# Kernel optimization log

Measured on AMD Instinct MI355X. Metric: run time of the kernel, lower is better.

Reference implementation:

```python
import jax, jax.numpy as jnp
import numpy as np

B, N, IN_DIM, OUT_DIM, C = 8, 8192, 1024, 512, 64
TEMPERATURE = 1.0
LN_EPS = 1e-5


def setup_inputs() -> dict:
    key = jax.random.key(0)
    ks = jax.random.split(key, 6)
    node_embeddings = jax.random.normal(ks[0], (B, N, IN_DIM), dtype=jnp.float32)
    node_mask = jnp.zeros((B, N), dtype=bool)  # True => node is masked out
    # xavier_uniform for cluster_centers [C, OUT_DIM]
    lim_c = float(np.sqrt(6.0 / (C + OUT_DIM)))
    cluster_centers = jax.random.uniform(ks[1], (C, OUT_DIM), jnp.float32, -lim_c, lim_c)
    # nn.Linear default init (kaiming-uniform-ish bounds)
    lim_n = float(1.0 / np.sqrt(IN_DIM))
    W_node = jax.random.uniform(ks[2], (IN_DIM, OUT_DIM), jnp.float32, -lim_n, lim_n)
    b_node = jax.random.uniform(ks[3], (OUT_DIM,), jnp.float32, -lim_n, lim_n)
    lim_k = float(1.0 / np.sqrt(OUT_DIM))
    W_cluster = jax.random.uniform(ks[4], (OUT_DIM, OUT_DIM), jnp.float32, -lim_k, lim_k)
    b_cluster = jax.random.uniform(ks[5], (OUT_DIM,), jnp.float32, -lim_k, lim_k)
    ln_gamma = jnp.ones((OUT_DIM,), jnp.float32)
    ln_beta = jnp.zeros((OUT_DIM,), jnp.float32)
    return {
        "node_embeddings": node_embeddings,
        "node_mask": node_mask,
        "cluster_centers": cluster_centers,
        "W_node": W_node,
        "b_node": b_node,
        "W_cluster": W_cluster,
        "b_cluster": b_cluster,
        "ln_gamma": ln_gamma,
        "ln_beta": ln_beta,
    }


def reference(node_embeddings, node_mask, cluster_centers, W_node, b_node,
              W_cluster, b_cluster, ln_gamma, ln_beta):
    # node projection: [B, N, D]
    node_proj = jnp.einsum('bni,io->bno', node_embeddings, W_node) + b_node
    # projected cluster centers (batch-independent): [C, D]
    ccp = cluster_centers @ W_cluster + b_cluster
    # similarities: [B, C, N]
    sims = jnp.einsum('cd,bnd->bcn', ccp, node_proj) / TEMPERATURE
    sims = jnp.where(node_mask[:, None, :], -jnp.inf, sims)
    assignment_weights = jax.nn.softmax(sims, axis=-1)  # dropout is identity in eval
    # aggregate: [B, C, D], residual add of projected centers
    compressed = jnp.einsum('bcn,bnd->bcd', assignment_weights, node_proj) + ccp
    # LayerNorm over last dim
    mu = jnp.mean(compressed, axis=-1, keepdims=True)
    var = jnp.var(compressed, axis=-1, keepdims=True)
    compressed = (compressed - mu) * jax.lax.rsqrt(var + LN_EPS) * ln_gamma + ln_beta
    return compressed, assignment_weights
```

## Files before the change

### kernel.cpp

```cpp
#include <hip/hip_runtime.h>
#include <hip/hip_bf16.h>
#include <math.h>

#define Bn 8
#define Nn 8192
#define KIN 1024
#define DOUT 512
#define NC 64
#define LN_EPS 1e-5f

typedef short bf16x8 __attribute__((ext_vector_type(8)));
typedef short s4v __attribute__((ext_vector_type(4)));
typedef short s8v __attribute__((ext_vector_type(8)));
typedef float f32x4 __attribute__((ext_vector_type(4)));

__device__ __forceinline__ short f2bf(float f) {
    __hip_bfloat16 h = __float2bfloat16(f);
    return __builtin_bit_cast(short, h);
}

__device__ __forceinline__ void load_lds16(const void* g, void* l) {
    __builtin_amdgcn_global_load_lds(
        (const __attribute__((address_space(1))) unsigned int*)g,
        (__attribute__((address_space(3))) unsigned int*)l, 16, 0, 0);
}

__global__ void k_prep_w(const float* __restrict__ W, short* __restrict__ Wt) {
    int o = blockIdx.x * 256 + threadIdx.x;
    int n = o >> 10, k = o & 1023;
    Wt[o] = f2bf(W[k * DOUT + n]);
}

__global__ void k_prep_c(const float* __restrict__ cc, const float* __restrict__ Wc,
                         const float* __restrict__ bc, float* __restrict__ ccp_f,
                         short* __restrict__ ccp_bf) {
    int o = blockIdx.x * 256 + threadIdx.x;
    int c = o >> 9, n = o & 511;
    float a = bc[n];
    for (int k = 0; k < DOUT; ++k) a += cc[c * DOUT + k] * Wc[k * DOUT + n];
    ccp_f[o] = a;
    ccp_bf[o] = f2bf(a);
}

__global__ __launch_bounds__(512) void k_gemm1(
    const float* __restrict__ A, const short* __restrict__ Wt,
    const float* __restrict__ bias, short* __restrict__ proj) {
    __shared__ short As[64 * 32];
    __shared__ short Bs[512 * 32];
    const int tid = threadIdx.x;
    const int lane = tid & 63, wv = tid >> 6;
    const int quad = lane >> 4, l15 = lane & 15;
    const int m0 = blockIdx.x * 64;

    f32x4 acc[4][4];
#pragma unroll
    for (int i = 0; i < 4; ++i)
#pragma unroll
        for (int j = 0; j < 4; ++j) acc[i][j] = (f32x4){0.f, 0.f, 0.f, 0.f};

    const int ar = tid >> 3;
    const int akq = (tid & 7) * 4;
    const float* Ag = A + (size_t)(m0 + ar) * KIN + akq;

    for (int it = 0; it < KIN / 32; ++it) {
        __syncthreads();
        const int k0 = it * 32;
        {
            float4 av = *reinterpret_cast<const float4*>(Ag + k0);
            s4v pv;
            pv.x = f2bf(av.x); pv.y = f2bf(av.y); pv.z = f2bf(av.z); pv.w = f2bf(av.w);
            *reinterpret_cast<s4v*>(&As[ar * 32 + akq]) = pv;
        }
#pragma unroll
        for (int iss = 0; iss < 4; ++iss) {
            int c = iss * 512 + tid;
            int n = c >> 2, kc = c & 3;
            load_lds16(Wt + n * KIN + k0 + kc * 8, Bs + (iss * 512 + wv * 64) * 8);
        }
        __syncthreads();
        bf16x8 af[4], bfr[4];
#pragma unroll
        for (int mi = 0; mi < 4; ++mi)
            af[mi] = *reinterpret_cast<const bf16x8*>(&As[(mi * 16 + l15) * 32 + quad * 8]);
#pragma unroll
        for (int ni = 0; ni < 4; ++ni)
            bfr[ni] = *reinterpret_cast<const bf16x8*>(&Bs[(wv * 64 + ni * 16 + l15) * 32 + quad * 8]);
#pragma unroll
        for (int mi = 0; mi < 4; ++mi)
#pragma unroll
            for (int ni = 0; ni < 4; ++ni)
                acc[mi][ni] = __builtin_amdgcn_mfma_f32_16x16x32_bf16(af[mi], bfr[ni], acc[mi][ni], 0, 0, 0);
    }
#pragma unroll
    for (int ni = 0; ni < 4; ++ni) {
        int col = wv * 64 + ni * 16 + l15;
        float bv = bias[col];
#pragma unroll
        for (int mi = 0; mi < 4; ++mi)
#pragma unroll
            for (int r = 0; r < 4; ++r) {
                int row = m0 + mi * 16 + quad * 4 + r;
                proj[(size_t)row * DOUT + col] = f2bf(acc[mi][ni][r] + bv);
            }
    }
}

__global__ __launch_bounds__(256) void k_sims(
    const short* __restrict__ ccp_bf, const short* __restrict__ proj,
    float* __restrict__ sims) {
    __shared__ short As[64 * 32];
    __shared__ short Bs[128 * 32];
    const int tid = threadIdx.x, lane = tid & 63, wv = tid >> 6;
    const int quad = lane >> 4, l15 = lane & 15;
    const int b = blockIdx.x >> 6, nt = blockIdx.x & 63;
    const int n0 = nt * 128;
    const int wm = wv >> 1, wn = wv & 1;

    f32x4 acc[2][4];
#pragma unroll
    for (int i = 0; i < 2; ++i)
#pragma unroll
        for (int j = 0; j < 4; ++j) acc[i][j] = (f32x4){0.f, 0.f, 0.f, 0.f};

    for (int it = 0; it < DOUT / 32; ++it) {
        __syncthreads();
        const int k0 = it * 32;
        {
            int r = tid >> 2, kc = tid & 3;
            load_lds16(ccp_bf + r * DOUT + k0 + kc * 8, As + wv * 64 * 8);
        }
#pragma unroll
        for (int iss = 0; iss < 2; ++iss) {
            int c = iss * 256 + tid;
            int r = c >> 2, kc = c & 3;
            load_lds16(proj + (size_t)(b * Nn + n0 + r) * DOUT + k0 + kc * 8,
                       Bs + (iss * 256 + wv * 64) * 8);
        }
        __syncthreads();
        bf16x8 af[2], bfr[4];
#pragma unroll
        for (int mi = 0; mi < 2; ++mi)
            af[mi] = *reinterpret_cast<const bf16x8*>(&As[(wm * 32 + mi * 16 + l15) * 32 + quad * 8]);
#pragma unroll
        for (int ni = 0; ni < 4; ++ni)
            bfr[ni] = *reinterpret_cast<const bf16x8*>(&Bs[(wn * 64 + ni * 16 + l15) * 32 + quad * 8]);
#pragma unroll
        for (int mi = 0; mi < 2; ++mi)
#pragma unroll
            for (int ni = 0; ni < 4; ++ni)
                acc[mi][ni] = __builtin_amdgcn_mfma_f32_16x16x32_bf16(af[mi], bfr[ni], acc[mi][ni], 0, 0, 0);
    }
#pragma unroll
    for (int mi = 0; mi < 2; ++mi)
#pragma unroll
        for (int ni = 0; ni < 4; ++ni)
#pragma unroll
            for (int r = 0; r < 4; ++r) {
                int c = wm * 32 + mi * 16 + quad * 4 + r;
                int n = n0 + wn * 64 + ni * 16 + l15;
                sims[((size_t)b * NC + c) * Nn + n] = acc[mi][ni][r];
            }
}

__global__ __launch_bounds__(256) void k_softmax(
    float* __restrict__ aw, const unsigned char* __restrict__ mask,
    short* __restrict__ aw_bf) {
    __shared__ float red[8];
    const int tid = threadIdx.x, lane = tid & 63, wv = tid >> 6;
    const int b = blockIdx.x >> 6, c = blockIdx.x & 63;
    float* p = aw + ((size_t)b * NC + c) * Nn;
    short* q = aw_bf + ((size_t)b * NC + c) * Nn;
    const unsigned char* mp = mask + b * Nn;

    float v[32];
    float mx = -INFINITY;
#pragma unroll
    for (int i = 0; i < 32; ++i) {
        int idx = tid + i * 256;
        float x = p[idx];
        if (mp[idx]) x = -INFINITY;
        v[i] = x;
        mx = fmaxf(mx, x);
    }
    for (int off = 32; off; off >>= 1) mx = fmaxf(mx, __shfl_xor(mx, off));
    if (lane == 0) red[wv] = mx;
    __syncthreads();
    mx = fmaxf(fmaxf(red[0], red[1]), fmaxf(red[2], red[3]));
    __syncthreads();

    float s = 0.f;
#pragma unroll
    for (int i = 0; i < 32; ++i) {
        v[i] = expf(v[i] - mx);
        s += v[i];
    }
    for (int off = 32; off; off >>= 1) s += __shfl_xor(s, off);
    if (lane == 0) red[wv] = s;
    __syncthreads();
    s = red[0] + red[1] + red[2] + red[3];
    float inv = 1.f / s;
#pragma unroll
    for (int i = 0; i < 32; ++i) {
        int idx = tid + i * 256;
        float w = v[i] * inv;
        p[idx] = w;
        q[idx] = f2bf(w);
    }
}

__global__ __launch_bounds__(256) void k_agg(
    const short* __restrict__ aw_bf, const short* __restrict__ proj,
    float* __restrict__ partial) {
    __shared__ short As[64 * 32];
    __shared__ short Bs[64 * 40];
    const int tid = threadIdx.x, lane = tid & 63, wv = tid >> 6;
    const int quad = lane >> 4, l15 = lane & 15;
    const int b = blockIdx.x >> 6, dt = (blockIdx.x >> 3) & 7, ks = blockIdx.x & 7;
    const int d0 = dt * 64;
    const int wc = wv >> 1, wd = wv & 1;

    f32x4 acc[2][2];
#pragma unroll
    for (int i = 0; i < 2; ++i)
#pragma unroll
        for (int j = 0; j < 2; ++j) acc[i][j] = (f32x4){0.f, 0.f, 0.f, 0.f};

    const int bk = tid >> 3;
    const int bj0 = (tid & 7) * 8;

    for (int it = 0; it < 32; ++it) {
        const int nb = ks * 1024 + it * 32;
        __syncthreads();
        {
            int r = tid >> 2, kc = tid & 3;
            load_lds16(aw_bf + ((size_t)b * NC + r) * Nn + nb + kc * 8, As + wv * 64 * 8);
        }
        {
            const short* g = proj + (size_t)(b * Nn + nb + bk) * DOUT + d0 + bj0;
            s8v x = *reinterpret_cast<const s8v*>(g);
#pragma unroll
            for (int j = 0; j < 8; ++j) Bs[(bj0 + j) * 40 + bk] = x[j];
        }
        __syncthreads();
        bf16x8 af[2], bfr[2];
#pragma unroll
        for (int ci = 0; ci < 2; ++ci)
            af[ci] = *reinterpret_cast<const bf16x8*>(&As[(wc * 32 + ci * 16 + l15) * 32 + quad * 8]);
#pragma unroll
        for (int di = 0; di < 2; ++di)
            bfr[di] = *reinterpret_cast<const bf16x8*>(&Bs[(wd * 32 + di * 16 + l15) * 40 + quad * 8]);
#pragma unroll
        for (int ci = 0; ci < 2; ++ci)
#pragma unroll
            for (int di = 0; di < 2; ++di)
                acc[ci][di] = __builtin_amdgcn_mfma_f32_16x16x32_bf16(af[ci], bfr[di], acc[ci][di], 0, 0, 0);
    }
#pragma unroll
    for (int ci = 0; ci < 2; ++ci)
#pragma unroll
        for (int di = 0; di < 2; ++di)
#pragma unroll
            for (int r = 0; r < 4; ++r) {
                int c = wc * 32 + ci * 16 + quad * 4 + r;
                int d = d0 + wd * 32 + di * 16 + l15;
                partial[(((size_t)b * 8 + ks) * NC + c) * DOUT + d] = acc[ci][di][r];
            }
}

__global__ __launch_bounds__(256) void k_ln(
    const float* __restrict__ partial, const float* __restrict__ ccp,
    const float* __restrict__ gamma, const float* __restrict__ beta,
    float* __restrict__ out) {
    __shared__ float red[16];
    const int tid = threadIdx.x, lane = tid & 63, wv = tid >> 6;
    const int b = blockIdx.x >> 6, c = blockIdx.x & 63;
    float v0 = ccp[c * DOUT + tid], v1 = ccp[c * DOUT + tid + 256];
#pragma unroll
    for (int ks = 0; ks < 8; ++ks) {
        const float* pp = partial + (((size_t)b * 8 + ks) * NC + c) * DOUT;
        v0 += pp[tid];
        v1 += pp[tid + 256];
    }
    float s = v0 + v1, sq = v0 * v0 + v1 * v1;
    for (int off = 32; off; off >>= 1) {
        s += __shfl_xor(s, off);
        sq += __shfl_xor(sq, off);
    }
    if (lane == 0) { red[wv] = s; red[8 + wv] = sq; }
    __syncthreads();
    s = red[0] + red[1] + red[2] + red[3];
    sq = red[8] + red[9] + red[10] + red[11];
    float mu = s * (1.f / 512.f);
    float var = sq * (1.f / 512.f) - mu * mu;
    float rs = rsqrtf(var + LN_EPS);
    size_t base = ((size_t)b * NC + c) * DOUT;
    out[base + tid] = (v0 - mu) * rs * gamma[tid] + beta[tid];
    out[base + tid + 256] = (v1 - mu) * rs * gamma[tid + 256] + beta[tid + 256];
}

extern "C" void kernel_launch(void* const* d_in, const int* in_sizes, int n_in,
                              void* d_out, int out_size, void* d_ws, size_t ws_size,
                              hipStream_t stream) {
    const float* node_emb = (const float*)d_in[0];
    const unsigned char* mask = (const unsigned char*)d_in[1];
    const float* cc = (const float*)d_in[2];
    const float* Wn = (const float*)d_in[3];
    const float* bn = (const float*)d_in[4];
    const float* Wc = (const float*)d_in[5];
    const float* bc = (const float*)d_in[6];
    const float* gamma = (const float*)d_in[7];
    const float* beta = (const float*)d_in[8];
    float* out = (float*)d_out;

    char* ws = (char*)d_ws;
    short* proj   = (short*)(ws);
    short* Wt     = (short*)(ws + 67108864);
    float* ccp_f  = (float*)(ws + 68157440);
    short* ccp_bf = (short*)(ws + 68288512);
    short* aw_bf  = (short*)(ws + 68354048);
    float* partial= (float*)(ws + 76742656);

    float* sims = out + (size_t)Bn * NC * DOUT;

    k_prep_w<<<2048, 256, 0, stream>>>(Wn, Wt);
    k_prep_c<<<128, 256, 0, stream>>>(cc, Wc, bc, ccp_f, ccp_bf);
    k_gemm1<<<1024, 512, 0, stream>>>(node_emb, Wt, bn, proj);
    k_sims<<<512, 256, 0, stream>>>(ccp_bf, proj, sims);
    k_softmax<<<512, 256, 0, stream>>>(sims, mask, aw_bf);
    k_agg<<<512, 256, 0, stream>>>(aw_bf, proj, partial);
    k_ln<<<512, 256, 0, stream>>>(partial, ccp_f, gamma, beta, out);
}
```

Baseline: 579.9 us.

## Retile projection GEMM, widen sims tiles, pre-transpose proj for aggregation

The projection GEMM moves from 64-row blocks covering all 512 outputs to 128x128 tiles with padded A rows in LDS. The sims kernel doubles its node tile to 256 with 512 threads. A new transpose kernel writes proj in d-major order so the aggregation kernel can use direct global-to-LDS loads with a 64-wide k step and 16-way split-K instead of scalar transposed LDS stores. This costs an extra 64 MB round trip through memory for projT and more partial sums to reduce in the LayerNorm kernel.

```diff
diff --git a/kernel.cpp b/kernel.cpp
--- a/kernel.cpp
+++ b/kernel.cpp
@@ -10,7 +10,6 @@
 #define LN_EPS 1e-5f
 
 typedef short bf16x8 __attribute__((ext_vector_type(8)));
-typedef short s4v __attribute__((ext_vector_type(4)));
 typedef short s8v __attribute__((ext_vector_type(8)));
 typedef float f32x4 __attribute__((ext_vector_type(4)));
 
@@ -42,15 +41,16 @@
     ccp_bf[o] = f2bf(a);
 }
 
-__global__ __launch_bounds__(512) void k_gemm1(
+__global__ __launch_bounds__(256) void k_gemm1(
     const float* __restrict__ A, const short* __restrict__ Wt,
     const float* __restrict__ bias, short* __restrict__ proj) {
-    __shared__ short As[64 * 32];
-    __shared__ short Bs[512 * 32];
-    const int tid = threadIdx.x;
-    const int lane = tid & 63, wv = tid >> 6;
+    __shared__ short As[128 * 40];
+    __shared__ short Bs[128 * 32];
+    const int tid = threadIdx.x, lane = tid & 63, wv = tid >> 6;
     const int quad = lane >> 4, l15 = lane & 15;
-    const int m0 = blockIdx.x * 64;
+    const int mt = blockIdx.x >> 2, nt = blockIdx.x & 3;
+    const int m0 = mt * 128, n0 = nt * 128;
+    const int wm = wv >> 1, wn = wv & 1;
 
     f32x4 acc[4][4];
 #pragma unroll
@@ -58,33 +58,41 @@
 #pragma unroll
         for (int j = 0; j < 4; ++j) acc[i][j] = (f32x4){0.f, 0.f, 0.f, 0.f};
 
-    const int ar = tid >> 3;
-    const int akq = (tid & 7) * 4;
-    const float* Ag = A + (size_t)(m0 + ar) * KIN + akq;
+    const int ar = tid >> 1;
+    const int ac = (tid & 1) * 16;
+    const float* Ag = A + (size_t)(m0 + ar) * KIN + ac;
 
     for (int it = 0; it < KIN / 32; ++it) {
-        __syncthreads();
         const int k0 = it * 32;
+        __syncthreads();
         {
-            float4 av = *reinterpret_cast<const float4*>(Ag + k0);
-            s4v pv;
-            pv.x = f2bf(av.x); pv.y = f2bf(av.y); pv.z = f2bf(av.z); pv.w = f2bf(av.w);
-            *reinterpret_cast<s4v*>(&As[ar * 32 + akq]) = pv;
-        }
-#pragma unroll
-        for (int iss = 0; iss < 4; ++iss) {
-            int c = iss * 512 + tid;
+            float4 a0 = *reinterpret_cast<const float4*>(Ag + k0);
+            float4 a1 = *reinterpret_cast<const float4*>(Ag + k0 + 4);
+            float4 a2 = *reinterpret_cast<const float4*>(Ag + k0 + 8);
+            float4 a3 = *reinterpret_cast<const float4*>(Ag + k0 + 12);
+            s8v p0, p1;
+            p0[0]=f2bf(a0.x); p0[1]=f2bf(a0.y); p0[2]=f2bf(a0.z); p0[3]=f2bf(a0.w);
+            p0[4]=f2bf(a1.x); p0[5]=f2bf(a1.y); p0[6]=f2bf(a1.z); p0[7]=f2bf(a1.w);
+            p1[0]=f2bf(a2.x); p1[1]=f2bf(a2.y); p1[2]=f2bf(a2.z); p1[3]=f2bf(a2.w);
+            p1[4]=f2bf(a3.x); p1[5]=f2bf(a3.y); p1[6]=f2bf(a3.z); p1[7]=f2bf(a3.w);
+            *reinterpret_cast<s8v*>(&As[ar * 40 + ac]) = p0;
+            *reinterpret_cast<s8v*>(&As[ar * 40 + ac + 8]) = p1;
+        }
+#pragma unroll
+        for (int i = 0; i < 2; ++i) {
+            int c = i * 256 + tid;
             int n = c >> 2, kc = c & 3;
-            load_lds16(Wt + n * KIN + k0 + kc * 8, Bs + (iss * 512 + wv * 64) * 8);
+            load_lds16(Wt + (size_t)(n0 + n) * KIN + k0 + kc * 8,
+                       Bs + (i * 256 + wv * 64) * 8);
         }
         __syncthreads();
         bf16x8 af[4], bfr[4];
 #pragma unroll
         for (int mi = 0; mi < 4; ++mi)
-            af[mi] = *reinterpret_cast<const bf16x8*>(&As[(mi * 16 + l15) * 32 + quad * 8]);
+            af[mi] = *reinterpret_cast<const bf16x8*>(&As[(wm * 64 + mi * 16 + l15) * 40 + quad * 8]);
 #pragma unroll
         for (int ni = 0; ni < 4; ++ni)
-            bfr[ni] = *reinterpret_cast<const bf16x8*>(&Bs[(wv * 64 + ni * 16 + l15) * 32 + quad * 8]);
+            bfr[ni] = *reinterpret_cast<const bf16x8*>(&Bs[(wn * 64 + ni * 16 + l15) * 32 + quad * 8]);
 #pragma unroll
         for (int mi = 0; mi < 4; ++mi)
 #pragma unroll
@@ -93,28 +101,28 @@
     }
 #pragma unroll
     for (int ni = 0; ni < 4; ++ni) {
-        int col = wv * 64 + ni * 16 + l15;
+        int col = n0 + wn * 64 + ni * 16 + l15;
         float bv = bias[col];
 #pragma unroll
         for (int mi = 0; mi < 4; ++mi)
 #pragma unroll
             for (int r = 0; r < 4; ++r) {
-                int row = m0 + mi * 16 + quad * 4 + r;
+                int row = m0 + wm * 64 + mi * 16 + quad * 4 + r;
                 proj[(size_t)row * DOUT + col] = f2bf(acc[mi][ni][r] + bv);
             }
     }
 }
 
-__global__ __launch_bounds__(256) void k_sims(
+__global__ __launch_bounds__(512) void k_sims(
     const short* __restrict__ ccp_bf, const short* __restrict__ proj,
     float* __restrict__ sims) {
     __shared__ short As[64 * 32];
-    __shared__ short Bs[128 * 32];
+    __shared__ short Bs[256 * 32];
     const int tid = threadIdx.x, lane = tid & 63, wv = tid >> 6;
     const int quad = lane >> 4, l15 = lane & 15;
-    const int b = blockIdx.x >> 6, nt = blockIdx.x & 63;
-    const int n0 = nt * 128;
-    const int wm = wv >> 1, wn = wv & 1;
+    const int b = blockIdx.x >> 5, nt = blockIdx.x & 31;
+    const int n0 = nt * 256;
+    const int wm = wv & 1, wn = wv >> 1;
 
     f32x4 acc[2][4];
 #pragma unroll
@@ -123,18 +131,18 @@
         for (int j = 0; j < 4; ++j) acc[i][j] = (f32x4){0.f, 0.f, 0.f, 0.f};
 
     for (int it = 0; it < DOUT / 32; ++it) {
-        __syncthreads();
         const int k0 = it * 32;
-        {
-            int r = tid >> 2, kc = tid & 3;
-            load_lds16(ccp_bf + r * DOUT + k0 + kc * 8, As + wv * 64 * 8);
-        }
-#pragma unroll
-        for (int iss = 0; iss < 2; ++iss) {
-            int c = iss * 256 + tid;
+        __syncthreads();
+        if (tid < 256) {
+            load_lds16(ccp_bf + (size_t)(tid >> 2) * DOUT + k0 + (tid & 3) * 8,
+                       As + (wv * 64) * 8);
+        }
+#pragma unroll
+        for (int i = 0; i < 2; ++i) {
+            int c = i * 512 + tid;
             int r = c >> 2, kc = c & 3;
             load_lds16(proj + (size_t)(b * Nn + n0 + r) * DOUT + k0 + kc * 8,
-                       Bs + (iss * 256 + wv * 64) * 8);
+                       Bs + (i * 512 + wv * 64) * 8);
         }
         __syncthreads();
         bf16x8 af[2], bfr[4];
@@ -208,62 +216,93 @@
     }
 }
 
+__global__ __launch_bounds__(256) void k_transpose(
+    const short* __restrict__ proj, short* __restrict__ projT) {
+    __shared__ short L[64 * 80];
+    const int tid = threadIdx.x;
+    const int nt = blockIdx.x >> 3, dt = blockIdx.x & 7;
+    {
+        int n = tid >> 2, d0 = (tid & 3) * 16;
+        const short* g = proj + (size_t)(nt * 64 + n) * DOUT + dt * 64 + d0;
+        s8v x0 = *reinterpret_cast<const s8v*>(g);
+        s8v x1 = *reinterpret_cast<const s8v*>(g + 8);
+        *reinterpret_cast<s8v*>(&L[n * 80 + d0]) = x0;
+        *reinterpret_cast<s8v*>(&L[n * 80 + d0 + 8]) = x1;
+    }
+    __syncthreads();
+    {
+        int d = tid & 63, n0 = (tid >> 6) * 16;
+        s8v y0, y1;
+#pragma unroll
+        for (int j = 0; j < 8; ++j) y0[j] = L[(n0 + j) * 80 + d];
+#pragma unroll
+        for (int j = 0; j < 8; ++j) y1[j] = L[(n0 + 8 + j) * 80 + d];
+        short* o = projT + (size_t)(dt * 64 + d) * (Bn * Nn) + nt * 64 + n0;
+        *reinterpret_cast<s8v*>(o) = y0;
+        *reinterpret_cast<s8v*>(o + 8) = y1;
+    }
+}
+
 __global__ __launch_bounds__(256) void k_agg(
-    const short* __restrict__ aw_bf, const short* __restrict__ proj,
+    const short* __restrict__ aw_bf, const short* __restrict__ projT,
     float* __restrict__ partial) {
-    __shared__ short As[64 * 32];
-    __shared__ short Bs[64 * 40];
+    __shared__ short As[64 * 64];
+    __shared__ short Bs[128 * 64];
     const int tid = threadIdx.x, lane = tid & 63, wv = tid >> 6;
     const int quad = lane >> 4, l15 = lane & 15;
-    const int b = blockIdx.x >> 6, dt = (blockIdx.x >> 3) & 7, ks = blockIdx.x & 7;
-    const int d0 = dt * 64;
-    const int wc = wv >> 1, wd = wv & 1;
-
-    f32x4 acc[2][2];
+    const int b = blockIdx.x >> 6, dt = (blockIdx.x >> 4) & 3, ks = blockIdx.x & 15;
+    const int d0 = dt * 128;
+    const int wm = wv >> 1, wn = wv & 1;
+
+    f32x4 acc[2][4];
 #pragma unroll
     for (int i = 0; i < 2; ++i)
 #pragma unroll
-        for (int j = 0; j < 2; ++j) acc[i][j] = (f32x4){0.f, 0.f, 0.f, 0.f};
-
-    const int bk = tid >> 3;
-    const int bj0 = (tid & 7) * 8;
-
-    for (int it = 0; it < 32; ++it) {
-        const int nb = ks * 1024 + it * 32;
-        __syncthreads();
-        {
-            int r = tid >> 2, kc = tid & 3;
-            load_lds16(aw_bf + ((size_t)b * NC + r) * Nn + nb + kc * 8, As + wv * 64 * 8);
-        }
-        {
-            const short* g = proj + (size_t)(b * Nn + nb + bk) * DOUT + d0 + bj0;
-            s8v x = *reinterpret_cast<const s8v*>(g);
-#pragma unroll
-            for (int j = 0; j < 8; ++j) Bs[(bj0 + j) * 40 + bk] = x[j];
-        }
-        __syncthreads();
-        bf16x8 af[2], bfr[2];
-#pragma unroll
-        for (int ci = 0; ci < 2; ++ci)
-            af[ci] = *reinterpret_cast<const bf16x8*>(&As[(wc * 32 + ci * 16 + l15) * 32 + quad * 8]);
-#pragma unroll
-        for (int di = 0; di < 2; ++di)
-            bfr[di] = *reinterpret_cast<const bf16x8*>(&Bs[(wd * 32 + di * 16 + l15) * 40 + quad * 8]);
-#pragma unroll
-        for (int ci = 0; ci < 2; ++ci)
-#pragma unroll
-            for (int di = 0; di < 2; ++di)
-                acc[ci][di] = __builtin_amdgcn_mfma_f32_16x16x32_bf16(af[ci], bfr[di], acc[ci][di], 0, 0, 0);
-    }
-#pragma unroll
-    for (int ci = 0; ci < 2; ++ci)
-#pragma unroll
-        for (int di = 0; di < 2; ++di)
+        for (int j = 0; j < 4; ++j) acc[i][j] = (f32x4){0.f, 0.f, 0.f, 0.f};
+
+    for (int it = 0; it < 8; ++it) {
+        const int nb = ks * 512 + it * 64;
+        __syncthreads();
+#pragma unroll
+        for (int i = 0; i < 2; ++i) {
+            int c = i * 256 + tid;
+            int r = c >> 3, kc = c & 7;
+            load_lds16(aw_bf + ((size_t)b * NC + r) * Nn + nb + kc * 8,
+                       As + (i * 256 + wv * 64) * 8);
+        }
+#pragma unroll
+        for (int i = 0; i < 4; ++i) {
+            int c = i * 256 + tid;
+            int r = c >> 3, kc = c & 7;
+            load_lds16(projT + (size_t)(d0 + r) * (Bn * Nn) + b * Nn + nb + kc * 8,
+                       Bs + (i * 256 + wv * 64) * 8);
+        }
+        __syncthreads();
+#pragma unroll
+        for (int k2 = 0; k2 < 2; ++k2) {
+            bf16x8 af[2], bfr[4];
+#pragma unroll
+            for (int mi = 0; mi < 2; ++mi)
+                af[mi] = *reinterpret_cast<const bf16x8*>(&As[(wm * 32 + mi * 16 + l15) * 64 + k2 * 32 + quad * 8]);
+#pragma unroll
+            for (int ni = 0; ni < 4; ++ni)
+                bfr[ni] = *reinterpret_cast<const bf16x8*>(&Bs[(wn * 64 + ni * 16 + l15) * 64 + k2 * 32 + quad * 8]);
+#pragma unroll
+            for (int mi = 0; mi < 2; ++mi)
+#pragma unroll
+                for (int ni = 0; ni < 4; ++ni)
+                    acc[mi][ni] = __builtin_amdgcn_mfma_f32_16x16x32_bf16(af[mi], bfr[ni], acc[mi][ni], 0, 0, 0);
+        }
+    }
+#pragma unroll
+    for (int mi = 0; mi < 2; ++mi)
+#pragma unroll
+        for (int ni = 0; ni < 4; ++ni)
 #pragma unroll
             for (int r = 0; r < 4; ++r) {
-                int c = wc * 32 + ci * 16 + quad * 4 + r;
-                int d = d0 + wd * 32 + di * 16 + l15;
-                partial[(((size_t)b * 8 + ks) * NC + c) * DOUT + d] = acc[ci][di][r];
+                int c = wm * 32 + mi * 16 + quad * 4 + r;
+                int d = d0 + wn * 64 + ni * 16 + l15;
+                partial[(((size_t)b * 16 + ks) * NC + c) * DOUT + d] = acc[mi][ni][r];
             }
 }
 
@@ -276,8 +315,8 @@
     const int b = blockIdx.x >> 6, c = blockIdx.x & 63;
     float v0 = ccp[c * DOUT + tid], v1 = ccp[c * DOUT + tid + 256];
 #pragma unroll
-    for (int ks = 0; ks < 8; ++ks) {
-        const float* pp = partial + (((size_t)b * 8 + ks) * NC + c) * DOUT;
+    for (int ks = 0; ks < 16; ++ks) {
+        const float* pp = partial + (((size_t)b * 16 + ks) * NC + c) * DOUT;
         v0 += pp[tid];
         v1 += pp[tid + 256];
     }
@@ -314,19 +353,21 @@
 
     char* ws = (char*)d_ws;
     short* proj   = (short*)(ws);
-    short* Wt     = (short*)(ws + 67108864);
-    float* ccp_f  = (float*)(ws + 68157440);
-    short* ccp_bf = (short*)(ws + 68288512);
-    short* aw_bf  = (short*)(ws + 68354048);
-    float* partial= (float*)(ws + 76742656);
+    short* projT  = (short*)(ws + 67108864);
+    short* aw_bf  = (short*)(ws + 134217728);
+    float* ccp_f  = (float*)(ws + 142606336);
+    short* ccp_bf = (short*)(ws + 142737408);
+    short* Wt     = (short*)(ws + 142802944);
+    float* partial= (float*)(ws + 143851520);
 
     float* sims = out + (size_t)Bn * NC * DOUT;
 
     k_prep_w<<<2048, 256, 0, stream>>>(Wn, Wt);
     k_prep_c<<<128, 256, 0, stream>>>(cc, Wc, bc, ccp_f, ccp_bf);
-    k_gemm1<<<1024, 512, 0, stream>>>(node_emb, Wt, bn, proj);
-    k_sims<<<512, 256, 0, stream>>>(ccp_bf, proj, sims);
+    k_gemm1<<<2048, 256, 0, stream>>>(node_emb, Wt, bn, proj);
+    k_sims<<<256, 512, 0, stream>>>(ccp_bf, proj, sims);
     k_softmax<<<512, 256, 0, stream>>>(sims, mask, aw_bf);
-    k_agg<<<512, 256, 0, stream>>>(aw_bf, proj, partial);
+    k_transpose<<<8192, 256, 0, stream>>>(proj, projT);
+    k_agg<<<512, 256, 0, stream>>>(aw_bf, projT, partial);
     k_ln<<<512, 256, 0, stream>>>(partial, ccp_f, gamma, beta, out);
 }
```

After: 594.7 us. 1.03x slower.
